# Kernel tuning notes

Measured on AMD Instinct MI355X. Metric: run time of the kernel, lower is better.

The kernel has to match this reference:

```python
import jax, jax.numpy as jnp
import numpy as np

L, B, N, D, H, DH, MLP = 4, 4, 2048, 512, 8, 64, 2048
EPS = 1e-5


def layer_norm(x, w, b):
    mu = jnp.mean(x, axis=-1, keepdims=True)
    var = jnp.mean(jnp.square(x - mu), axis=-1, keepdims=True)
    return (x - mu) * jax.lax.rsqrt(var + EPS) * w + b


def setup_inputs() -> dict:
    key = jax.random.key(0)
    ks = jax.random.split(key, 8)
    x = jax.random.normal(ks[0], (B, N, D), dtype=jnp.float32)
    # mask == 1.0 means blocked: triu(ones) - eye -> strict upper triangle
    mask = jnp.triu(jnp.ones((N, N), dtype=jnp.float32)) - jnp.eye(N, dtype=jnp.float32)
    s = 0.02
    return {
        "x": x,
        "mask": mask,
        "ln1_w": jnp.ones((L, D), jnp.float32),
        "ln1_b": jnp.zeros((L, D), jnp.float32),
        "w_qkv": jax.random.normal(ks[1], (L, D, 3 * H * DH), jnp.float32) * s,
        "w_out": jax.random.normal(ks[2], (L, H * DH, D), jnp.float32) * s,
        "b_out": jnp.zeros((L, D), jnp.float32),
        "ln2_w": jnp.ones((L, D), jnp.float32),
        "ln2_b": jnp.zeros((L, D), jnp.float32),
        "w1": jax.random.normal(ks[3], (L, D, MLP), jnp.float32) * s,
        "b1": jnp.zeros((L, MLP), jnp.float32),
        "w2": jax.random.normal(ks[4], (L, MLP, D), jnp.float32) * s,
        "b2": jnp.zeros((L, D), jnp.float32),
    }


def reference(x, mask, ln1_w, ln1_b, w_qkv, w_out, b_out, ln2_w, ln2_b, w1, b1, w2, b2):
    scale = DH ** (-0.5)
    blocked = (mask == 1.0)  # [N, N]
    for l in range(L):
        # --- masked self-attention (pre-norm) ---
        h = layer_norm(x, ln1_w[l], ln1_b[l])
        qkv = h @ w_qkv[l]                               # [B, N, 3*H*DH]
        q, k, v = jnp.split(qkv, 3, axis=-1)
        q = q.reshape(B, N, H, DH).transpose(0, 2, 1, 3)  # bhnd
        k = k.reshape(B, N, H, DH).transpose(0, 2, 1, 3)
        v = v.reshape(B, N, H, DH).transpose(0, 2, 1, 3)
        scores = jnp.einsum('bhnd,bhmd->bhnm', q, k) * scale
        scores = jnp.where(blocked, -jnp.inf, scores)
        att = jax.nn.softmax(scores, axis=-1)
        o = jnp.einsum('bhnm,bhmd->bhnd', att, v)
        o = o.transpose(0, 2, 1, 3).reshape(B, N, H * DH)
        x = x + (o @ w_out[l] + b_out[l])
        # --- GELU MLP (pre-norm) ---
        h2 = layer_norm(x, ln2_w[l], ln2_b[l])
        ff = jax.nn.gelu(h2 @ w1[l] + b1[l], approximate=False) @ w2[l] + b2[l]
        x = x + ff
    return x
```

## Files before the change

### kernel.cpp

```cpp
#include <hip/hip_runtime.h>
#include <math.h>

#define L 4
#define BATCH 4
#define N 2048
#define D 512
#define H 8
#define DH 64
#define MLPD 2048
#define M_ROWS (BATCH * N)
#define VTP 2064

using v8s = __attribute__((ext_vector_type(8))) short;
using v4f = __attribute__((ext_vector_type(4))) float;

__device__ inline short f2bf(float f) {
  union { float f; unsigned u; } v; v.f = f;
  unsigned r = v.u + 0x7FFFu + ((v.u >> 16) & 1u);
  return (short)(r >> 16);
}
__device__ inline unsigned pack2bf_t(float a, float b) {
  union { float f; unsigned u; } x, y; x.f = a; y.f = b;
  return (x.u >> 16) | (y.u & 0xFFFF0000u);
}

#define MFMA(a, b, c) __builtin_amdgcn_mfma_f32_16x16x32_bf16(a, b, c, 0, 0, 0)

__device__ __forceinline__ void gload_lds16(const void* g, void* l) {
  __builtin_amdgcn_global_load_lds((const __attribute__((address_space(1))) void*)g,
                                   (__attribute__((address_space(3))) void*)l, 16, 0, 0);
}

__global__ void copyf4_kernel(const float4* __restrict__ in, float4* __restrict__ out, int n) {
  int i = blockIdx.x * blockDim.x + threadIdx.x;
  if (i < n) out[i] = in[i];
}

__launch_bounds__(256)
__global__ void transpose_w_kernel(const float* __restrict__ src, short* __restrict__ dst,
                                   int R, int C) {
  __shared__ float tile[32][33];
  const size_t base = (size_t)blockIdx.z * R * C;
  const int c0 = blockIdx.x * 32, r0 = blockIdx.y * 32;
  const int tx = threadIdx.x & 31, ty = threadIdx.x >> 5;
  #pragma unroll
  for (int i = ty; i < 32; i += 8)
    tile[i][tx] = src[base + (size_t)(r0 + i) * C + c0 + tx];
  __syncthreads();
  #pragma unroll
  for (int i = ty; i < 32; i += 8)
    dst[base + (size_t)(c0 + i) * R + r0 + tx] = f2bf(tile[tx][i]);
}

__launch_bounds__(256)
__global__ void ln_kernel(const float* __restrict__ x, const float* __restrict__ w,
                          const float* __restrict__ b, short* __restrict__ out) {
  const int row = blockIdx.x * 4 + (threadIdx.x >> 6);
  const int lane = threadIdx.x & 63;
  const float* xr = x + (size_t)row * D;
  float4 a0 = *(const float4*)(xr + lane * 8);
  float4 a1 = *(const float4*)(xr + lane * 8 + 4);
  float v[8] = {a0.x, a0.y, a0.z, a0.w, a1.x, a1.y, a1.z, a1.w};
  float s = 0.f;
  #pragma unroll
  for (int j = 0; j < 8; ++j) s += v[j];
  #pragma unroll
  for (int m = 1; m < 64; m <<= 1) s += __shfl_xor(s, m, 64);
  const float mean = s * (1.0f / D);
  float q = 0.f;
  #pragma unroll
  for (int j = 0; j < 8; ++j) { float d = v[j] - mean; q += d * d; }
  #pragma unroll
  for (int m = 1; m < 64; m <<= 1) q += __shfl_xor(q, m, 64);
  const float rstd = rsqrtf(q * (1.0f / D) + 1e-5f);
  float4 w0 = *(const float4*)(w + lane * 8);
  float4 w1 = *(const float4*)(w + lane * 8 + 4);
  float4 b0 = *(const float4*)(b + lane * 8);
  float4 b1 = *(const float4*)(b + lane * 8 + 4);
  float wv[8] = {w0.x, w0.y, w0.z, w0.w, w1.x, w1.y, w1.z, w1.w};
  float bv[8] = {b0.x, b0.y, b0.z, b0.w, b1.x, b1.y, b1.z, b1.w};
  v8s r;
  #pragma unroll
  for (int j = 0; j < 8; ++j) r[j] = f2bf((v[j] - mean) * rstd * wv[j] + bv[j]);
  *(v8s*)(out + (size_t)row * D + lane * 8) = r;
}

template <int MODE, int BN>
__launch_bounds__(256)
__global__ void gemm128_kernel(const short* __restrict__ A, const short* __restrict__ Bt,
                               const float* __restrict__ bias, const float* __restrict__ Xres,
                               void* __restrict__ Out, int M, int Nc, int K) {
  constexpr int MR = (BN == 128) ? 4 : 2;
  __shared__ __align__(16) short As[2][128 * 64];
  __shared__ __align__(16) short Bs[2][BN * 64];
  const int tid = threadIdx.x;
  const int lane = tid & 63;
  const int w = tid >> 6;
  const int wr = (BN == 128) ? (w >> 1) : w;
  const int wc = (BN == 128) ? (w & 1) : 0;
  const int r16 = lane & 15, g = lane >> 4;

  const int nxb = Nc / BN;
  const int nyb = M >> 7;
  const int bid = (int)blockIdx.x;
  const int xcd = bid & 7;
  const int ii = bid >> 3;
  const int byi = xcd * (nyb >> 3) + ii / nxb;
  const int bxi = ii % nxb;
  const int m0 = byi * 128, n0 = bxi * BN;

  const int srow = lane >> 3;
  const int ssw = ((lane & 7) ^ srow) * 8;

  auto STAGE = [&](int buf, int k0) {
    #pragma unroll
    for (int j = 0; j < 4; ++j) {
      const int row = w * 32 + j * 8;
      gload_lds16(A + (size_t)(m0 + row + srow) * K + k0 + ssw,
                  (char*)&As[buf][0] + row * 128);
    }
    #pragma unroll
    for (int j = 0; j < BN / 32; ++j) {
      const int row = w * (BN / 4) + j * 8;
      gload_lds16(Bt + (size_t)(n0 + row + srow) * K + k0 + ssw,
                  (char*)&Bs[buf][0] + row * 128);
    }
  };

  v4f acc[MR][4] = {};

  STAGE(0, 0);
  __syncthreads();
  int cur = 0;
  for (int k0 = 0; k0 < K; k0 += 64) {
    if (k0 + 64 < K) STAGE(cur ^ 1, k0 + 64);
    v8s af[MR][2], bf[4][2];
    #pragma unroll
    for (int m = 0; m < MR; ++m) {
      const int row = wr * (MR * 16) + m * 16 + r16;
      #pragma unroll
      for (int kh = 0; kh < 2; ++kh)
        af[m][kh] = *(const v8s*)((const char*)&As[cur][0] + row * 128 +
                                  (((kh * 4 + g) ^ (row & 7)) * 16));
    }
    #pragma unroll
    for (int n = 0; n < 4; ++n) {
      const int row = wc * 64 + n * 16 + r16;
      #pragma unroll
      for (int kh = 0; kh < 2; ++kh)
        bf[n][kh] = *(const v8s*)((const char*)&Bs[cur][0] + row * 128 +
                                  (((kh * 4 + g) ^ (row & 7)) * 16));
    }
    #pragma unroll
    for (int kh = 0; kh < 2; ++kh)
      #pragma unroll
      for (int m = 0; m < MR; ++m)
        #pragma unroll
        for (int n = 0; n < 4; ++n)
          acc[m][n] = MFMA(af[m][kh], bf[n][kh], acc[m][n]);
    __syncthreads();
    cur ^= 1;
  }

  #pragma unroll
  for (int m = 0; m < MR; ++m) {
    const int row = m0 + wr * (MR * 16) + m * 16 + g * 4;
    #pragma unroll
    for (int n = 0; n < 4; ++n) {
      const int col = n0 + wc * 64 + n * 16 + r16;
      const float bv = bias ? bias[col] : 0.0f;
      #pragma unroll
      for (int r = 0; r < 4; ++r) {
        const size_t idx = (size_t)(row + r) * Nc + col;
        float val = acc[m][n][r] + bv;
        if constexpr (MODE == 0) {
          ((short*)Out)[idx] = f2bf(val);
        } else if constexpr (MODE == 1) {
          const float z = val * 0.70710678118f;
          const float az = fabsf(z);
          const float t = 1.0f / (1.0f + 0.3275911f * az);
          const float p =
              0.254829592f +
              t * (-0.284496736f + t * (1.421413741f + t * (-1.453152027f + t * 1.061405429f)));
          float er = 1.0f - p * t * __expf(-az * az);
          er = (z < 0.0f) ? -er : er;
          val = 0.5f * val * (1.0f + er);
          ((short*)Out)[idx] = f2bf(val);
        } else {
          ((float*)Out)[idx] = val + Xres[idx];
        }
      }
    }
  }
}

__launch_bounds__(256)
__global__ void kv_prep_kernel(const short* __restrict__ qkv, short* __restrict__ Vt) {
  __shared__ __align__(16) short tile[64][88];
  const int b = blockIdx.z, h = blockIdx.y, n0 = blockIdx.x * 64;
  const int tid = threadIdx.x;
  const int bh = b * H + h;
  const int row2 = tid >> 3, d0 = (tid & 7) * 8;
  #pragma unroll
  for (int i = 0; i < 2; ++i) {
    const int n = i * 32 + row2;
    const short* src = qkv + ((size_t)(b * N + n0 + n)) * 1536 + 1024 + h * 64 + d0;
    *(v8s*)&tile[n][d0] = *(const v8s*)src;
  }
  __syncthreads();
  const int dh = tid & 63, nc = (tid >> 6) * 16;
  #pragma unroll
  for (int j = 0; j < 2; ++j) {
    const int oc = nc + j * 8;
    const int base = (oc >> 5) * 32 + ((oc >> 3) & 3) * 4;
    v8s ov;
    #pragma unroll
    for (int e = 0; e < 4; ++e) ov[e] = tile[base + e][dh];
    #pragma unroll
    for (int e = 0; e < 4; ++e) ov[4 + e] = tile[base + 16 + e][dh];
    *(v8s*)(Vt + ((size_t)(bh * 64 + dh)) * VTP + n0 + oc) = ov;
  }
}

__launch_bounds__(256)
__global__ void attn_kernel(const short* __restrict__ qkv, const short* __restrict__ Vt,
                            short* __restrict__ o) {
  __shared__ __align__(16) short Ks[2][64 * 64];
  __shared__ __align__(16) short Vs[2][64 * 64];
  const int lin = (int)blockIdx.x;
  const int bh = ((lin >> 3) & 3) * 8 + (lin & 7);
  const int xl2 = 31 - (lin >> 5);
  const int b = bh >> 3, h = bh & 7;
  const int q0 = xl2 * 64;
  const int tid = threadIdx.x, lane = tid & 63, w = tid >> 6;
  const int r16 = lane & 15, g = lane >> 4;
  const int qw = q0 + w * 16;

  v8s qf0, qf1;
  {
    const size_t qbase = ((size_t)(b * N + qw + r16)) * 1536 + h * 64;
    qf0 = *(const v8s*)(qkv + qbase + g * 8);
    qf1 = *(const v8s*)(qkv + qbase + 32 + g * 8);
  }

  const short* vtb = Vt + (size_t)bh * 64 * VTP;

  const int srow = lane >> 3;
  const int ssw = ((lane & 7) ^ srow) * 8;

  v4f oacc[4] = {};
  float lsum = 0.f;
  const int tdiag = xl2;

  auto STAGE = [&](int buf, int t) {
    const int k0 = t * 64;
    #pragma unroll
    for (int j = 0; j < 2; ++j) {
      const int row = w * 16 + j * 8 + srow;
      gload_lds16(qkv + ((size_t)(b * N + k0 + row)) * 1536 + 512 + h * 64 + ssw,
                  (char*)&Ks[buf][0] + (w * 16 + j * 8) * 128);
      gload_lds16(vtb + (size_t)row * VTP + k0 + ssw,
                  (char*)&Vs[buf][0] + (w * 16 + j * 8) * 128);
    }
  };

  STAGE(0, 0);
  __syncthreads();
  int cur = 0;
  for (int t = 0; t <= tdiag; ++t) {
    if (t < tdiag) STAGE(cur ^ 1, t + 1);
    const int k0 = t * 64;
    const char* kb = (const char*)&Ks[cur][0];
    const char* vb = (const char*)&Vs[cur][0];

    v8s vf[4][2];
    #pragma unroll
    for (int a = 0; a < 4; ++a)
      #pragma unroll
      for (int c = 0; c < 2; ++c)
        vf[a][c] = *(const v8s*)(vb + (a * 16 + r16) * 128 + (((c * 4 + g) ^ (r16 & 7)) * 16));

    __builtin_amdgcn_s_setprio(1);
    v4f s[4];
    #pragma unroll
    for (int kt = 0; kt < 4; ++kt) {
      const int krow = (kt * 16 + r16) * 128;
      v8s kfa = *(const v8s*)(kb + krow + ((g ^ (r16 & 7)) * 16));
      v8s kfb = *(const v8s*)(kb + krow + (((4 + g) ^ (r16 & 7)) * 16));
      v4f ss = {};
      ss = MFMA(kfa, qf0, ss);
      ss = MFMA(kfb, qf1, ss);
      s[kt] = ss;
    }
    __builtin_amdgcn_s_setprio(0);

    const bool needmask = (t == tdiag);
    const int qrow = qw + r16;
    const int kbase = k0 + 4 * g;
    unsigned pw_[8];
    #pragma unroll
    for (int kt = 0; kt < 4; ++kt) {
      float e[4];
      #pragma unroll
      for (int r = 0; r < 4; ++r) {
        float v = s[kt][r] * 0.125f;
        if (needmask && (kbase + kt * 16 + r > qrow)) v = -3e38f;
        e[r] = __expf(v);
      }
      lsum += (e[0] + e[1]) + (e[2] + e[3]);
      pw_[kt * 2 + 0] = pack2bf_t(e[0], e[1]);
      pw_[kt * 2 + 1] = pack2bf_t(e[2], e[3]);
    }
    union PU { unsigned u[4]; v8s s8; };
    PU pa0, pa1;
    pa0.u[0] = pw_[0]; pa0.u[1] = pw_[1]; pa0.u[2] = pw_[2]; pa0.u[3] = pw_[3];
    pa1.u[0] = pw_[4]; pa1.u[1] = pw_[5]; pa1.u[2] = pw_[6]; pa1.u[3] = pw_[7];

    __builtin_amdgcn_s_setprio(1);
    #pragma unroll
    for (int dt = 0; dt < 4; ++dt) oacc[dt] = MFMA(pa0.s8, vf[dt][0], oacc[dt]);
    #pragma unroll
    for (int dt = 0; dt < 4; ++dt) oacc[dt] = MFMA(pa1.s8, vf[dt][1], oacc[dt]);
    __builtin_amdgcn_s_setprio(0);

    __syncthreads();
    cur ^= 1;
  }

  lsum += __shfl_xor(lsum, 16, 64);
  lsum += __shfl_xor(lsum, 32, 64);
  float ldiv[4];
  #pragma unroll
  for (int r = 0; r < 4; ++r) ldiv[r] = __shfl(lsum, g * 4 + r, 64);

  #pragma unroll
  for (int dt = 0; dt < 4; ++dt)
    #pragma unroll
    for (int r = 0; r < 4; ++r) {
      const float val = oacc[dt][r] / ldiv[r];
      o[((size_t)(b * N + qw + g * 4 + r)) * 512 + h * 64 + dt * 16 + r16] = f2bf(val);
    }
}

extern "C" void kernel_launch(void* const* d_in, const int* in_sizes, int n_in,
                              void* d_out, int out_size, void* d_ws, size_t ws_size,
                              hipStream_t stream) {
  const float* x_in  = (const float*)d_in[0];
  const float* ln1_w = (const float*)d_in[2];
  const float* ln1_b = (const float*)d_in[3];
  const float* w_qkv = (const float*)d_in[4];
  const float* w_out = (const float*)d_in[5];
  const float* b_out = (const float*)d_in[6];
  const float* ln2_w = (const float*)d_in[7];
  const float* ln2_b = (const float*)d_in[8];
  const float* w1    = (const float*)d_in[9];
  const float* b1    = (const float*)d_in[10];
  const float* w2    = (const float*)d_in[11];
  const float* b2    = (const float*)d_in[12];

  char* ws = (char*)d_ws;
  size_t off = 0;
  auto alloc = [&](size_t bytes) { char* p = ws + off; off += (bytes + 255) & ~(size_t)255; return p; };
  short* wqkvT = (short*)alloc((size_t)L * 1536 * 512 * 2);
  short* woutT = (short*)alloc((size_t)L * 512 * 512 * 2);
  short* w1T   = (short*)alloc((size_t)L * 512 * 2048 * 2);
  short* w2T   = (short*)alloc((size_t)L * 2048 * 512 * 2);
  short* hln   = (short*)alloc((size_t)M_ROWS * 512 * 2);
  short* big   = (short*)alloc((size_t)M_ROWS * 2048 * 2);
  short* oatt  = (short*)alloc((size_t)M_ROWS * 512 * 2);
  short* Vtg   = (short*)alloc((size_t)BATCH * H * 64 * VTP * 2);
  short* qkv = big;
  short* ff  = big;

  float* x = (float*)d_out;

  copyf4_kernel<<<4096, 256, 0, stream>>>((const float4*)x_in, (float4*)x, M_ROWS * D / 4);

  transpose_w_kernel<<<dim3(1536 / 32, 512 / 32, L), 256, 0, stream>>>(w_qkv, wqkvT, 512, 1536);
  transpose_w_kernel<<<dim3(512 / 32, 512 / 32, L), 256, 0, stream>>>(w_out, woutT, 512, 512);
  transpose_w_kernel<<<dim3(2048 / 32, 512 / 32, L), 256, 0, stream>>>(w1, w1T, 512, 2048);
  transpose_w_kernel<<<dim3(512 / 32, 2048 / 32, L), 256, 0, stream>>>(w2, w2T, 2048, 512);

  for (int l = 0; l < L; ++l) {
    ln_kernel<<<M_ROWS / 4, 256, 0, stream>>>(x, ln1_w + l * 512, ln1_b + l * 512, hln);
    gemm128_kernel<0, 128><<<dim3((1536 / 128) * (M_ROWS / 128)), 256, 0, stream>>>(
        hln, wqkvT + (size_t)l * 1536 * 512, nullptr, nullptr, qkv, M_ROWS, 1536, 512);
    kv_prep_kernel<<<dim3(N / 64, H, BATCH), 256, 0, stream>>>(qkv, Vtg);
    attn_kernel<<<dim3(1024), 256, 0, stream>>>(qkv, Vtg, oatt);
    gemm128_kernel<2, 64><<<dim3((512 / 64) * (M_ROWS / 128)), 256, 0, stream>>>(
        oatt, woutT + (size_t)l * 512 * 512, b_out + l * 512, x, x, M_ROWS, 512, 512);
    ln_kernel<<<M_ROWS / 4, 256, 0, stream>>>(x, ln2_w + l * 512, ln2_b + l * 512, hln);
    gemm128_kernel<1, 128><<<dim3((2048 / 128) * (M_ROWS / 128)), 256, 0, stream>>>(
        hln, w1T + (size_t)l * 512 * 2048, b1 + l * 2048, nullptr, ff, M_ROWS, 2048, 512);
    gemm128_kernel<2, 64><<<dim3((512 / 64) * (M_ROWS / 128)), 256, 0, stream>>>(
        ff, w2T + (size_t)l * 2048 * 512, b2 + l * 512, x, x, M_ROWS, 512, 2048);
  }
}
```

Baseline: 674.2 us.

## Add 256x256-tile 8-wave GEMM with quadrant ping-pong pipeline for QKV and MLP-up

Adds a new GEMM kernel with 256x256 output tiles, 512 threads and a 4-slot LDS ring fed by direct global-to-LDS loads. The K loop is split into quadrant MMA phases, with barriers, waitcnts and setprio interleaving loads and MFMAs. Blocks are also remapped so each XCD handles its own group of row tiles. It is used for the QKV projection and the MLP-up with GELU, aiming at more operand reuse per tile and better load/compute overlap. The cost is heavy register and LDS use, plus scalar bf16 stores in the epilogue.

Result: faster. 628.9 us (-6.7%).

```diff
diff --git a/kernel.cpp b/kernel.cpp
--- a/kernel.cpp
+++ b/kernel.cpp
@@ -30,6 +30,10 @@
   __builtin_amdgcn_global_load_lds((const __attribute__((address_space(1))) void*)g,
                                    (__attribute__((address_space(3))) void*)l, 16, 0, 0);
 }
+
+#define FENCE asm volatile("" ::: "memory")
+#define BAR  do { FENCE; __builtin_amdgcn_s_barrier(); FENCE; } while (0)
+#define VMW(n) asm volatile("s_waitcnt vmcnt(" #n ")" ::: "memory")
 
 __global__ void copyf4_kernel(const float4* __restrict__ in, float4* __restrict__ out, int n) {
   int i = blockIdx.x * blockDim.x + threadIdx.x;
@@ -83,6 +87,161 @@
   #pragma unroll
   for (int j = 0; j < 8; ++j) r[j] = f2bf((v[j] - mean) * rstd * wv[j] + bv[j]);
   *(v8s*)(out + (size_t)row * D + lane * 8) = r;
+}
+
+template <int MODE, int NT>
+__launch_bounds__(512, 2)
+__global__ void gemm256_kernel(const short* __restrict__ A, const short* __restrict__ Bt,
+                               const float* __restrict__ bias, void* __restrict__ Out,
+                               int M, int Nc) {
+  constexpr int K = NT * 64;
+  __shared__ __align__(16) short Ah[4][128 * 64];
+  __shared__ __align__(16) short Bh[4][128 * 64];
+  const int tid = threadIdx.x, lane = tid & 63, w = tid >> 6;
+  const int wr = w >> 2, wc = w & 3;
+  const int r16 = lane & 15, g = lane >> 4;
+
+  const int nxb = Nc >> 8;
+  const int nyb = M >> 8;
+  const int bid = (int)blockIdx.x;
+  const int xcd = bid & 7, ii = bid >> 3;
+  const int byi = xcd * (nyb >> 3) + ii / nxb;
+  const int bxi = ii % nxb;
+  const int m0 = byi << 8, n0 = bxi << 8;
+
+  const int srow = lane >> 3;
+  const int ssw = ((lane & 7) ^ srow) * 8;
+
+  const short* Abase = A + (size_t)(m0 + srow) * K + ssw;
+  const short* Bbase = Bt + (size_t)(n0 + srow) * K + ssw;
+
+  auto STAGE_A = [&](int j) {
+    if (j >= 2 * NT) return;
+    const int slot = j & 3, k0 = (j >> 1) * 64, r0 = (j & 1) * 128;
+    #pragma unroll
+    for (int i = 0; i < 2; ++i) {
+      const int rr = i * 64 + w * 8;
+      gload_lds16(Abase + (size_t)(r0 + rr) * K + k0, (char*)&Ah[slot][0] + rr * 128);
+    }
+  };
+  auto STAGE_B = [&](int j) {
+    if (j >= 2 * NT) return;
+    const int slot = j & 3, k0 = (j >> 1) * 64, c0 = (j & 1) * 128;
+    #pragma unroll
+    for (int i = 0; i < 2; ++i) {
+      const int rr = i * 64 + w * 8;
+      gload_lds16(Bbase + (size_t)(c0 + rr) * K + k0, (char*)&Bh[slot][0] + rr * 128);
+    }
+  };
+
+  const int arow = wr * 64 + r16;
+  const int brow = wc * 32 + r16;
+  const int swz7 = r16 & 7;
+
+  v8s ar[4][2], br0[2][2], br1[2][2];
+  auto LDA = [&](int slot) {
+    const char* base = (const char*)&Ah[slot][0];
+    #pragma unroll
+    for (int mf = 0; mf < 4; ++mf)
+      #pragma unroll
+      for (int kh = 0; kh < 2; ++kh)
+        ar[mf][kh] = *(const v8s*)(base + (arow + mf * 16) * 128 + (((kh * 4 + g) ^ swz7) * 16));
+  };
+  auto LDB0 = [&](int slot) {
+    const char* base = (const char*)&Bh[slot][0];
+    #pragma unroll
+    for (int nf = 0; nf < 2; ++nf)
+      #pragma unroll
+      for (int kh = 0; kh < 2; ++kh)
+        br0[nf][kh] = *(const v8s*)(base + (brow + nf * 16) * 128 + (((kh * 4 + g) ^ swz7) * 16));
+  };
+  auto LDB1 = [&](int slot) {
+    const char* base = (const char*)&Bh[slot][0];
+    #pragma unroll
+    for (int nf = 0; nf < 2; ++nf)
+      #pragma unroll
+      for (int kh = 0; kh < 2; ++kh)
+        br1[nf][kh] = *(const v8s*)(base + (brow + nf * 16) * 128 + (((kh * 4 + g) ^ swz7) * 16));
+  };
+
+  v4f acc[2][2][4][2] = {};
+
+#define MMA_Q(QM, QN, BR)                                                      \
+  do {                                                                         \
+    __builtin_amdgcn_s_setprio(1);                                             \
+    _Pragma("unroll")                                                          \
+    for (int kh = 0; kh < 2; ++kh)                                             \
+      _Pragma("unroll")                                                        \
+      for (int mf = 0; mf < 4; ++mf)                                           \
+        _Pragma("unroll")                                                      \
+        for (int nf = 0; nf < 2; ++nf)                                         \
+          acc[QM][QN][mf][nf] = MFMA(ar[mf][kh], BR[nf][kh], acc[QM][QN][mf][nf]); \
+    __builtin_amdgcn_s_setprio(0);                                             \
+  } while (0)
+
+  STAGE_A(0); STAGE_B(0); STAGE_B(1); STAGE_A(1); STAGE_A(2); STAGE_B(2); STAGE_B(3);
+  VMW(6);
+  BAR;
+
+  auto KTILE = [&](int T, int sa) {
+    LDA(sa); LDB0(sa);
+    STAGE_A(2 * T + 3);
+    BAR;
+    MMA_Q(0, 0, br0);
+    BAR;
+    LDB1(sa + 1);
+    BAR;
+    MMA_Q(0, 1, br1);
+    BAR;
+    LDA(sa + 1);
+    STAGE_A(2 * T + 4); STAGE_B(2 * T + 4);
+    BAR;
+    MMA_Q(1, 1, br1);
+    BAR;
+    STAGE_B(2 * T + 5);
+    BAR;
+    MMA_Q(1, 0, br0);
+    VMW(4);
+    BAR;
+  };
+
+  #pragma unroll
+  for (int t2 = 0; t2 < NT / 2; ++t2) {
+    KTILE(2 * t2, 0);
+    KTILE(2 * t2 + 1, 2);
+  }
+#undef MMA_Q
+
+  #pragma unroll
+  for (int qm = 0; qm < 2; ++qm)
+    #pragma unroll
+    for (int mf = 0; mf < 4; ++mf) {
+      const int row = m0 + qm * 128 + wr * 64 + mf * 16 + g * 4;
+      #pragma unroll
+      for (int qn = 0; qn < 2; ++qn)
+        #pragma unroll
+        for (int nf = 0; nf < 2; ++nf) {
+          const int col = n0 + qn * 128 + wc * 32 + nf * 16 + r16;
+          float bv = 0.0f;
+          if constexpr (MODE == 1) bv = bias[col];
+          #pragma unroll
+          for (int r = 0; r < 4; ++r) {
+            float val = acc[qm][qn][mf][nf][r] + bv;
+            if constexpr (MODE == 1) {
+              const float z = val * 0.70710678118f;
+              const float az = fabsf(z);
+              const float t = 1.0f / (1.0f + 0.3275911f * az);
+              const float p =
+                  0.254829592f +
+                  t * (-0.284496736f + t * (1.421413741f + t * (-1.453152027f + t * 1.061405429f)));
+              float er = 1.0f - p * t * __expf(-az * az);
+              er = (z < 0.0f) ? -er : er;
+              val = 0.5f * val * (1.0f + er);
+            }
+            ((short*)Out)[(size_t)(row + r) * Nc + col] = f2bf(val);
+          }
+        }
+    }
 }
 
 template <int MODE, int BN>
@@ -383,15 +542,15 @@
 
   for (int l = 0; l < L; ++l) {
     ln_kernel<<<M_ROWS / 4, 256, 0, stream>>>(x, ln1_w + l * 512, ln1_b + l * 512, hln);
-    gemm128_kernel<0, 128><<<dim3((1536 / 128) * (M_ROWS / 128)), 256, 0, stream>>>(
-        hln, wqkvT + (size_t)l * 1536 * 512, nullptr, nullptr, qkv, M_ROWS, 1536, 512);
+    gemm256_kernel<0, 8><<<dim3((1536 / 256) * (M_ROWS / 256)), 512, 0, stream>>>(
+        hln, wqkvT + (size_t)l * 1536 * 512, nullptr, qkv, M_ROWS, 1536);
     kv_prep_kernel<<<dim3(N / 64, H, BATCH), 256, 0, stream>>>(qkv, Vtg);
     attn_kernel<<<dim3(1024), 256, 0, stream>>>(qkv, Vtg, oatt);
     gemm128_kernel<2, 64><<<dim3((512 / 64) * (M_ROWS / 128)), 256, 0, stream>>>(
         oatt, woutT + (size_t)l * 512 * 512, b_out + l * 512, x, x, M_ROWS, 512, 512);
     ln_kernel<<<M_ROWS / 4, 256, 0, stream>>>(x, ln2_w + l * 512, ln2_b + l * 512, hln);
-    gemm128_kernel<1, 128><<<dim3((2048 / 128) * (M_ROWS / 128)), 256, 0, stream>>>(
-        hln, w1T + (size_t)l * 512 * 2048, b1 + l * 2048, nullptr, ff, M_ROWS, 2048, 512);
+    gemm256_kernel<1, 8><<<dim3((2048 / 256) * (M_ROWS / 256)), 512, 0, stream>>>(
+        hln, w1T + (size_t)l * 512 * 2048, b1 + l * 2048, ff, M_ROWS, 2048);
     gemm128_kernel<2, 64><<<dim3((512 / 64) * (M_ROWS / 128)), 256, 0, stream>>>(
         ff, w2T + (size_t)l * 2048 * 512, b2 + l * 512, x, x, M_ROWS, 512, 2048);
   }
```
